# Kernel optimization log

Hardware: AMD Instinct MI355X
Metric: run time of the kernel (lower is better)

## Reference

```python
import jax, jax.numpy as jnp
import numpy as np

B, C, H, W = 8, 512, 64, 64
TEMB = 512
HIDDEN = 1024  # int(C * prompt_hidden_ratio=2.0)
K = C // 2     # max(1, int(C * topk_ratio=0.5))


def silu(x):
    return x * jax.nn.sigmoid(x)


def conv1x1(h, w, b):
    # h: [b,c,hh,ww], w: [out,in], b: [out]
    return jnp.einsum('bchw,oc->bohw', h, w) + b[None, :, None, None]


def setup_inputs() -> dict:
    key = jax.random.key(0)
    ks = jax.random.split(key, 12)
    s = 0.02  # small init so softmax/attention stay well-conditioned
    return {
        'x': jax.random.normal(ks[0], (B, C, H, W), jnp.float32),
        'temb': jax.random.normal(ks[1], (B, TEMB), jnp.float32),
        'w_affine': jax.random.normal(ks[2], (2 * C, TEMB), jnp.float32) * s,
        'b_affine': jnp.zeros((2 * C,), jnp.float32),
        'w_tp': jax.random.normal(ks[3], (C, TEMB), jnp.float32) * s,
        'b_tp': jnp.zeros((C,), jnp.float32),
        'w_m1': jax.random.normal(ks[4], (HIDDEN, 2 * C), jnp.float32) * s,
        'b_m1': jnp.zeros((HIDDEN,), jnp.float32),
        'w_m2': jax.random.normal(ks[5], (C, HIDDEN), jnp.float32) * s,
        'b_m2': jnp.zeros((C,), jnp.float32),
        'wq': jax.random.normal(ks[6], (C, C), jnp.float32) * s,
        'bq': jnp.zeros((C,), jnp.float32),
        'wk': jax.random.normal(ks[7], (C, C), jnp.float32) * s,
        'bk': jnp.zeros((C,), jnp.float32),
        'wv': jax.random.normal(ks[8], (C, C), jnp.float32) * s,
        'bv': jnp.zeros((C,), jnp.float32),
        'wo': jax.random.normal(ks[9], (C, C), jnp.float32) * s,
        'bo': jnp.zeros((C,), jnp.float32),
    }


def reference(x, temb, w_affine, b_affine, w_tp, b_tp, w_m1, b_m1, w_m2, b_m2,
              wq, bq, wk, bk, wv, bv, wo, bo):
    b, c, hgt, wgt = x.shape
    hw = hgt * wgt

    # TimeScaleShift
    temb_act = silu(temb)
    ss = temb_act @ w_affine.T + b_affine              # [b, 2c]
    scale, shift = jnp.split(ss, 2, axis=1)
    h = x * (1.0 + scale[:, :, None, None]) + shift[:, :, None, None]

    # channel prompt
    gap = h.mean(axis=(2, 3))                          # [b, c]
    time_prompt = temb_act @ w_tp.T + b_tp             # [b, c]
    pm = jnp.concatenate([gap, time_prompt], axis=1)   # [b, 2c]
    prompt = silu(pm @ w_m1.T + b_m1) @ w_m2.T + b_m2  # [b, c]

    # top-k channel selection
    _, topk_idx = jax.lax.top_k(prompt, K)             # [b, K] int32

    # q/k/v 1x1 convs, then gather selected channels
    qf = conv1x1(h, wq, bq).reshape(b, c, hw)
    kf = conv1x1(h, wk, bk).reshape(b, c, hw)
    vf = conv1x1(h, wv, bv).reshape(b, c, hw)
    idx3 = topk_idx[:, :, None]
    q = jnp.take_along_axis(qf, idx3, axis=1)          # [b, K, hw]
    k_feat = jnp.take_along_axis(kf, idx3, axis=1)
    v = jnp.take_along_axis(vf, idx3, axis=1)

    # channel attention on the selected subset
    attn = jnp.einsum('bkn,bln->bkl', q, k_feat) * (K ** -0.5)  # [b, K, K]
    attn = jax.nn.softmax(attn, axis=2)
    out = jnp.einsum('bkl,bln->bkn', attn, v)                   # [b, K, hw]

    # scatter back into a zero tensor at the selected channels
    out_full = jax.vmap(
        lambda o, i: jnp.zeros((c, hw), o.dtype).at[i].set(o)
    )(out, topk_idx).reshape(b, c, hgt, wgt)

    return conv1x1(out_full, wo, bo)
```

## Files before the change

### kernel.cpp

```cpp
#include <hip/hip_runtime.h>
#include <hip/hip_bf16.h>
#include <math.h>

typedef __hip_bfloat16 bf16;
typedef __bf16 bf16x8 __attribute__((ext_vector_type(8)));
typedef float f32x4 __attribute__((ext_vector_type(4)));

static __device__ __forceinline__ float b2f(bf16 v) { return __bfloat162float(v); }
static __device__ __forceinline__ bf16 f2b(float v) { return __float2bfloat16(v); }

#define GLOAD16(g, l) __builtin_amdgcn_global_load_lds( \
    (const __attribute__((address_space(1))) void*)(g), \
    (__attribute__((address_space(3))) void*)(l), 16, 0, 0)

#define TM 128
#define TN 64
#define TK 32

template <typename TOUT>
__global__ __launch_bounds__(256) void gemm_bt(
    const bf16* __restrict__ A, size_t sA,
    const bf16* __restrict__ Bt, size_t sB,
    const float* __restrict__ bias, size_t sBias, int hasBias,
    TOUT* __restrict__ D, size_t sD,
    int M, int N, int Kd, int transStore, int NXB)
{
    const int id = blockIdx.x;
    const int bz = id & 7;
    const int slot = id >> 3;
    const int bx = slot % NXB, by = slot / NXB;

    A  += (size_t)bz * sA;
    Bt += (size_t)bz * sB;
    D  += (size_t)bz * sD;
    if (hasBias) bias += (size_t)bz * sBias;

    const int m0 = by * TM, n0 = bx * TN;
    const int t = threadIdx.x, wv = t >> 6, lane = t & 63;
    const int lr = lane & 15, quad = lane >> 4;

    __shared__ bf16 lA[TM * TK];
    __shared__ bf16 lB[TN * TK];

    f32x4 acc[2][4];
#pragma unroll
    for (int i = 0; i < 2; ++i)
#pragma unroll
        for (int j = 0; j < 4; ++j) acc[i][j] = (f32x4){0.f, 0.f, 0.f, 0.f};

    const int srow = lane >> 2, scol = (lane & 3) * 8;
    const bf16* as0 = A  + (size_t)(m0 + wv * 16 + srow) * Kd + scol;
    const bf16* bs0 = Bt + (size_t)(n0 + wv * 16 + srow) * Kd + scol;
    bf16* la0 = lA + wv * 512;
    bf16* lb0 = lB + wv * 512;

    for (int k0 = 0; k0 < Kd; k0 += TK) {
        __syncthreads();
        GLOAD16(as0 + k0, la0);
        GLOAD16(as0 + (size_t)64 * Kd + k0, la0 + 2048);
        GLOAD16(bs0 + k0, lb0);
        __syncthreads();

        bf16x8 af0 = *(const bf16x8*)(lA + (wv * 32 + lr) * 32 + quad * 8);
        bf16x8 af1 = *(const bf16x8*)(lA + (wv * 32 + 16 + lr) * 32 + quad * 8);
#pragma unroll
        for (int j = 0; j < 4; ++j) {
            bf16x8 bfj = *(const bf16x8*)(lB + (j * 16 + lr) * 32 + quad * 8);
            acc[0][j] = __builtin_amdgcn_mfma_f32_16x16x32_bf16(af0, bfj, acc[0][j], 0, 0, 0);
            acc[1][j] = __builtin_amdgcn_mfma_f32_16x16x32_bf16(af1, bfj, acc[1][j], 0, 0, 0);
        }
    }

#pragma unroll
    for (int i = 0; i < 2; ++i) {
        const int mb = m0 + wv * 32 + i * 16 + quad * 4;
#pragma unroll
        for (int r = 0; r < 4; ++r) {
            const int mm = mb + r;
            const float bvv = hasBias ? bias[mm] : 0.f;
#pragma unroll
            for (int j = 0; j < 4; ++j) {
                const int nn = n0 + j * 16 + lr;
                const float v = acc[i][j][r] + bvv;
                const size_t o = transStore ? ((size_t)nn * M + mm)
                                            : ((size_t)mm * N + nn);
                if constexpr (__is_same(TOUT, float)) D[o] = v;
                else                                  D[o] = f2b(v);
            }
        }
    }
}

__global__ __launch_bounds__(256) void k_prep(const float* __restrict__ x,
                                              bf16* __restrict__ xT,
                                              float* __restrict__ xsump)
{
    const int b = blockIdx.z;
    const int c0 = blockIdx.y * 64;
    const int n0 = blockIdx.x * 512;
    const int t = threadIdx.x;
    const int cr = t >> 2;
    const int sub = t & 3;
    __shared__ bf16 tile[64][72];

    const float* xrow = x + ((size_t)b * 512 + c0 + cr) * 4096 + n0 + sub * 16;
    float s = 0.f;

    for (int st = 0; st < 8; ++st) {
        __syncthreads();
        float4 f[4];
#pragma unroll
        for (int q = 0; q < 4; ++q) f[q] = *(const float4*)(xrow + st * 64 + q * 4);
#pragma unroll
        for (int q = 0; q < 4; ++q) {
            s += f[q].x + f[q].y + f[q].z + f[q].w;
            union { bf16 h[4]; uint2 u; } p;
            p.h[0] = f2b(f[q].x); p.h[1] = f2b(f[q].y);
            p.h[2] = f2b(f[q].z); p.h[3] = f2b(f[q].w);
            *(uint2*)&tile[cr][sub * 16 + q * 4] = p.u;
        }
        __syncthreads();
        union { bf16 h[8]; uint4 u; } o0, o1;
#pragma unroll
        for (int i = 0; i < 8; ++i) o0.h[i] = tile[sub * 16 + i][cr];
#pragma unroll
        for (int i = 0; i < 8; ++i) o1.h[i] = tile[sub * 16 + 8 + i][cr];
        bf16* orow = xT + ((size_t)b * 4096 + n0 + st * 64 + cr) * 512 + c0 + sub * 16;
        *(uint4*)(orow)     = o0.u;
        *(uint4*)(orow + 8) = o1.u;
    }
    s += __shfl_down(s, 2);
    s += __shfl_down(s, 1);
    if (sub == 0) xsump[(size_t)blockIdx.x * 4096 + b * 512 + c0 + cr] = s;
}

__global__ __launch_bounds__(256) void gemm_qkv2(
    const bf16* __restrict__ Aall, const bf16* __restrict__ xT,
    const float* __restrict__ bias,
    bf16* __restrict__ qb, bf16* __restrict__ kb, bf16* __restrict__ vT)
{
    const int id = blockIdx.x;
    const int b = id & 7;
    const int slot = id >> 3;
    const int mt = slot % 6;
    const int n0 = (slot / 6) * 128;

    const bf16* A  = Aall + (size_t)b * 393216 + (size_t)mt * 65536;
    const bf16* Bt = xT + (size_t)b * 2097152;
    bias += b * 768 + mt * 128;

    const int t = threadIdx.x, w = t >> 6, lane = t & 63;
    const int lr = lane & 15, quad = lane >> 4;
    const int wr = w >> 1, wc = w & 1;

    __shared__ bf16 lA[128 * 32];
    __shared__ bf16 lB[128 * 32];

    f32x4 acc[4][4];
#pragma unroll
    for (int i = 0; i < 4; ++i)
#pragma unroll
        for (int j = 0; j < 4; ++j) acc[i][j] = (f32x4){0.f, 0.f, 0.f, 0.f};

    const int srow = lane >> 2, scol = (lane & 3) * 8;
    const bf16* as0 = A  + (size_t)(w * 16 + srow) * 512 + scol;
    const bf16* bs0 = Bt + (size_t)(n0 + w * 16 + srow) * 512 + scol;
    bf16* la0 = lA + w * 512;
    bf16* lb0 = lB + w * 512;

    for (int k0 = 0; k0 < 512; k0 += 32) {
        __syncthreads();
        GLOAD16(as0 + k0, la0);
        GLOAD16(as0 + 32768 + k0, la0 + 2048);
        GLOAD16(bs0 + k0, lb0);
        GLOAD16(bs0 + 32768 + k0, lb0 + 2048);
        __syncthreads();

        bf16x8 af[4], bfr[4];
#pragma unroll
        for (int i = 0; i < 4; ++i)
            af[i] = *(const bf16x8*)(lA + (wr * 64 + i * 16 + lr) * 32 + quad * 8);
#pragma unroll
        for (int j = 0; j < 4; ++j)
            bfr[j] = *(const bf16x8*)(lB + (wc * 64 + j * 16 + lr) * 32 + quad * 8);
#pragma unroll
        for (int i = 0; i < 4; ++i)
#pragma unroll
            for (int j = 0; j < 4; ++j)
                acc[i][j] = __builtin_amdgcn_mfma_f32_16x16x32_bf16(af[i], bfr[j], acc[i][j], 0, 0, 0);
    }

#pragma unroll
    for (int i = 0; i < 4; ++i) {
        const int mq = wr * 64 + i * 16 + quad * 4;
#pragma unroll
        for (int r = 0; r < 4; ++r) {
            const int ml = mq + r;
            const float bvv = bias[ml];
            const int mmg = mt * 128 + ml;
            const int mloc = mmg & 255;
#pragma unroll
            for (int j = 0; j < 4; ++j) {
                const int nn = n0 + wc * 64 + j * 16 + lr;
                const float v = acc[i][j][r] + bvv;
                if (mmg < 256)      qb[(size_t)b * 1048576 + (size_t)mloc * 4096 + nn] = f2b(v);
                else if (mmg < 512) kb[(size_t)b * 1048576 + (size_t)mloc * 4096 + nn] = f2b(v);
                else                vT[(size_t)b * 1048576 + (size_t)nn * 256 + mloc] = f2b(v);
            }
        }
    }
}

__global__ __launch_bounds__(256) void gemm_s_splitk(
    const bf16* __restrict__ qb, const bf16* __restrict__ kb,
    float* __restrict__ part)
{
    const int id = blockIdx.x;
    const int b = id & 7;
    const int slot = id >> 3;
    const int s = slot >> 3;
    const int rem = slot & 7;
    const int m0 = (rem >> 2) * TM, n0 = (rem & 3) * TN;

    const bf16* A  = qb + (size_t)b * 1048576;
    const bf16* Bt = kb + (size_t)b * 1048576;

    const int t = threadIdx.x, wv = t >> 6, lane = t & 63;
    const int lr = lane & 15, quad = lane >> 4;

    __shared__ bf16 lA[TM * TK];
    __shared__ bf16 lB[TN * TK];

    f32x4 acc[2][4];
#pragma unroll
    for (int i = 0; i < 2; ++i)
#pragma unroll
        for (int j = 0; j < 4; ++j) acc[i][j] = (f32x4){0.f, 0.f, 0.f, 0.f};

    const int srow = lane >> 2, scol = (lane & 3) * 8;
    const bf16* as0 = A  + (size_t)(m0 + wv * 16 + srow) * 4096 + scol;
    const bf16* bs0 = Bt + (size_t)(n0 + wv * 16 + srow) * 4096 + scol;
    bf16* la0 = lA + wv * 512;
    bf16* lb0 = lB + wv * 512;

    const int kBeg = s * 512, kEnd = kBeg + 512;
    for (int k0 = kBeg; k0 < kEnd; k0 += TK) {
        __syncthreads();
        GLOAD16(as0 + k0, la0);
        GLOAD16(as0 + (size_t)64 * 4096 + k0, la0 + 2048);
        GLOAD16(bs0 + k0, lb0);
        __syncthreads();

        bf16x8 af0 = *(const bf16x8*)(lA + (wv * 32 + lr) * 32 + quad * 8);
        bf16x8 af1 = *(const bf16x8*)(lA + (wv * 32 + 16 + lr) * 32 + quad * 8);
#pragma unroll
        for (int j = 0; j < 4; ++j) {
            bf16x8 bfj = *(const bf16x8*)(lB + (j * 16 + lr) * 32 + quad * 8);
            acc[0][j] = __builtin_amdgcn_mfma_f32_16x16x32_bf16(af0, bfj, acc[0][j], 0, 0, 0);
            acc[1][j] = __builtin_amdgcn_mfma_f32_16x16x32_bf16(af1, bfj, acc[1][j], 0, 0, 0);
        }
    }

    float* dst = part + ((size_t)(s * 8 + b) * 256) * 256;
#pragma unroll
    for (int i = 0; i < 2; ++i) {
        const int mb = m0 + wv * 32 + i * 16 + quad * 4;
#pragma unroll
        for (int r = 0; r < 4; ++r) {
            const int mm = mb + r;
#pragma unroll
            for (int j = 0; j < 4; ++j)
                dst[(size_t)mm * 256 + n0 + j * 16 + lr] = acc[i][j][r];
        }
    }
}


__global__ void k_silu(const float* __restrict__ in, float* __restrict__ out, int n)
{
    int i = blockIdx.x * 256 + threadIdx.x;
    if (i < n) {
        float v = in[i];
        out[i] = v / (1.f + expf(-v));
    }
}

__global__ void k_smallgemm(const float* __restrict__ in, const float* __restrict__ W,
                            const float* __restrict__ bias, float* __restrict__ out,
                            int Mrows, int O, int Kd, int act)
{
    const int gw = (blockIdx.x * 256 + threadIdx.x) >> 6;
    const int lane = threadIdx.x & 63;
    if (gw >= Mrows * O) return;
    const int m = gw / O, o = gw - m * O;
    float s = 0.f;
    for (int k = lane; k < Kd; k += 64)
        s += in[m * Kd + k] * W[(size_t)o * Kd + k];
    for (int off = 32; off; off >>= 1) s += __shfl_down(s, off);
    if (lane == 0) {
        s += bias[o];
        if (act) s = s / (1.f + expf(-s));
        out[m * O + o] = s;
    }
}

__global__ void k_mlp1(const float* __restrict__ ss, const float* __restrict__ xsump,
                       const float* __restrict__ tp, const float* __restrict__ w_m1,
                       const float* __restrict__ b_m1, float* __restrict__ hidden)
{
    const int gw = (blockIdx.x * 256 + threadIdx.x) >> 6;
    const int lane = threadIdx.x & 63;
    if (gw >= 8 * 1024) return;
    const int m = gw >> 10, o = gw & 1023;
    float s = 0.f;
    for (int k = lane; k < 1024; k += 64) {
        float pv;
        if (k < 512) {
            float xs = 0.f;
#pragma unroll
            for (int p = 0; p < 8; ++p) xs += xsump[p * 4096 + m * 512 + k];
            pv = (1.f + ss[m * 1024 + k]) * (xs * (1.f / 4096.f))
                 + ss[m * 1024 + 512 + k];
        } else {
            pv = tp[m * 512 + k - 512];
        }
        s += pv * w_m1[(size_t)o * 1024 + k];
    }
    for (int off = 32; off; off >>= 1) s += __shfl_down(s, off);
    if (lane == 0) {
        s += b_m1[o];
        hidden[m * 1024 + o] = s / (1.f + expf(-s));
    }
}

__global__ void k_topk(const float* __restrict__ prompt, int* __restrict__ idx)
{
    __shared__ float v[512];
    __shared__ int sel[512];
    const int b = blockIdx.x, c = threadIdx.x;
    v[c] = prompt[b * 512 + c];
    __syncthreads();
    const float mv = v[c];
    int rank = 0;
    for (int j = 0; j < 512; ++j) {
        float o = v[j];
        rank += (o > mv) || (o == mv && j < c);
    }
    sel[c] = (rank < 256) ? 1 : 0;
    __syncthreads();
    if (rank < 256) {
        int pos = 0;
        for (int j = 0; j < c; ++j) pos += sel[j];
        idx[b * 256 + pos] = c;
    }
}

__global__ void k_gather(const int* __restrict__ idx, const float* __restrict__ ss,
                         const float* __restrict__ wq, const float* __restrict__ wk,
                         const float* __restrict__ wv, const float* __restrict__ wo,
                         bf16* __restrict__ wqkv_g, bf16* __restrict__ wo_g)
{
    const int b = blockIdx.z;
    const int* id = idx + b * 256;
    const int tid = blockIdx.x * 256 + threadIdx.x;
    {
        const int mat = tid >> 17, r = tid & 131071;
        const int j = r >> 9, c = r & 511;
        const int ch = id[j];
        const float* W = mat == 0 ? wq : (mat == 1 ? wk : wv);
        wqkv_g[(size_t)b * 393216 + tid] = f2b(W[ch * 512 + c] * (1.f + ss[b * 1024 + c]));
    }
    if (tid < 131072) {
        const int o = tid >> 8, j = tid & 255;
        wo_g[(size_t)b * 131072 + tid] = f2b(wo[o * 512 + id[j]]);
    }
}

__global__ void k_biasadj(const int* __restrict__ idx, const float* __restrict__ ss,
                          const float* __restrict__ wq, const float* __restrict__ bq,
                          const float* __restrict__ wk, const float* __restrict__ bk,
                          const float* __restrict__ wv, const float* __restrict__ bv,
                          float* __restrict__ bqkv)
{
    const int gw = (blockIdx.x * 256 + threadIdx.x) >> 6;
    const int lane = threadIdx.x & 63;
    if (gw >= 8 * 768) return;
    const int b = gw / 768, j3 = gw - b * 768;
    const int mat = j3 >> 8, j = j3 & 255;
    const int ch = idx[b * 256 + j];
    const float* W  = mat == 0 ? wq : (mat == 1 ? wk : wv);
    const float* Bb = mat == 0 ? bq : (mat == 1 ? bk : bv);
    const float* shift = ss + b * 1024 + 512;
    float s = 0.f;
    for (int c = lane; c < 512; c += 64)
        s += W[(size_t)ch * 512 + c] * shift[c];
    for (int off = 32; off; off >>= 1) s += __shfl_down(s, off);
    if (lane == 0) bqkv[b * 768 + j3] = Bb[ch] + s;
}

__global__ void k_softmax_red(const float* __restrict__ part, bf16* __restrict__ Pt)
{
    const int row = blockIdx.x;
    const int b = row >> 8, j = row & 255;
    const int t = threadIdx.x;
    const int lane = t & 63, wv = t >> 6;
    __shared__ float redm[4], reds[4];
    float v = 0.f;
#pragma unroll
    for (int s = 0; s < 8; ++s)
        v += part[((size_t)(s * 8 + b) * 256 + j) * 256 + t];
    v *= 0.0625f;
    float m = v;
    for (int off = 32; off; off >>= 1) m = fmaxf(m, __shfl_down(m, off));
    if (lane == 0) redm[wv] = m;
    __syncthreads();
    m = fmaxf(fmaxf(redm[0], redm[1]), fmaxf(redm[2], redm[3]));
    const float e = __expf(v - m);
    float s = e;
    for (int off = 32; off; off >>= 1) s += __shfl_down(s, off);
    if (lane == 0) reds[wv] = s;
    __syncthreads();
    s = reds[0] + reds[1] + reds[2] + reds[3];
    Pt[(size_t)b * 65536 + (size_t)t * 256 + j] = f2b(e / s);
}


extern "C" void kernel_launch(void* const* d_in, const int* in_sizes, int n_in,
                              void* d_out, int out_size, void* d_ws, size_t ws_size,
                              hipStream_t stream)
{
    const float* x        = (const float*)d_in[0];
    const float* temb     = (const float*)d_in[1];
    const float* w_affine = (const float*)d_in[2];
    const float* b_affine = (const float*)d_in[3];
    const float* w_tp     = (const float*)d_in[4];
    const float* b_tp     = (const float*)d_in[5];
    const float* w_m1     = (const float*)d_in[6];
    const float* b_m1     = (const float*)d_in[7];
    const float* w_m2     = (const float*)d_in[8];
    const float* b_m2     = (const float*)d_in[9];
    const float* wq       = (const float*)d_in[10];
    const float* bq       = (const float*)d_in[11];
    const float* wk       = (const float*)d_in[12];
    const float* bk       = (const float*)d_in[13];
    const float* wv       = (const float*)d_in[14];
    const float* bv       = (const float*)d_in[15];
    const float* wo       = (const float*)d_in[16];
    const float* bo       = (const float*)d_in[17];
    float* out = (float*)d_out;

    char* ws = (char*)d_ws;
    size_t off = 0;
    auto alloc = [&](size_t bytes) -> char* {
        char* p = ws + off;
        off += (bytes + 255) & ~(size_t)255;
        return p;
    };

    float* temb_act = (float*)alloc(4096 * 4);
    float* ssb      = (float*)alloc(8192 * 4);
    float* tp       = (float*)alloc(4096 * 4);
    float* xsump    = (float*)alloc((size_t)8 * 4096 * 4);
    float* hidden   = (float*)alloc(8192 * 4);
    float* prompt   = (float*)alloc(4096 * 4);
    int*   idx      = (int*)alloc(2048 * 4);
    bf16*  xT     = (bf16*)alloc((size_t)8 * 4096 * 512 * 2);
    float* part   = (float*)alloc((size_t)8 * 8 * 256 * 256 * 4);
    bf16*  wqkv_g = (bf16*)alloc((size_t)8 * 768 * 512 * 2);
    float* bqkv_g = (float*)alloc(8 * 768 * 4);
    bf16*  wo_g   = (bf16*)alloc((size_t)8 * 512 * 256 * 2);
    bf16*  qb     = (bf16*)alloc((size_t)8 * 256 * 4096 * 2);
    bf16*  kb     = (bf16*)alloc((size_t)8 * 256 * 4096 * 2);
    bf16*  vT     = (bf16*)alloc((size_t)8 * 4096 * 256 * 2);
    bf16*  Pt     = (bf16*)alloc((size_t)8 * 256 * 256 * 2);
    bf16*  W2     = (bf16*)alloc((size_t)8 * 512 * 256 * 2);
    (void)ws_size; (void)n_in; (void)in_sizes; (void)out_size;

    k_prep<<<dim3(8, 8, 8), 256, 0, stream>>>(x, xT, xsump);
    k_silu<<<16, 256, 0, stream>>>(temb, temb_act, 4096);
    k_smallgemm<<<2048, 256, 0, stream>>>(temb_act, w_affine, b_affine, ssb, 8, 1024, 512, 0);
    k_smallgemm<<<1024, 256, 0, stream>>>(temb_act, w_tp, b_tp, tp, 8, 512, 512, 0);
    k_mlp1<<<2048, 256, 0, stream>>>(ssb, xsump, tp, w_m1, b_m1, hidden);
    k_smallgemm<<<1024, 256, 0, stream>>>(hidden, w_m2, b_m2, prompt, 8, 512, 1024, 0);
    k_topk<<<8, 512, 0, stream>>>(prompt, idx);
    k_gather<<<dim3(1536, 1, 8), 256, 0, stream>>>(idx, ssb, wq, wk, wv, wo, wqkv_g, wo_g);
    k_biasadj<<<1536, 256, 0, stream>>>(idx, ssb, wq, bq, wk, bk, wv, bv, bqkv_g);
    gemm_qkv2<<<1536, 256, 0, stream>>>(wqkv_g, xT, bqkv_g, qb, kb, vT);
    gemm_s_splitk<<<512, 256, 0, stream>>>(qb, kb, part);
    k_softmax_red<<<2048, 256, 0, stream>>>(part, Pt);
    gemm_bt<bf16><<<128, 256, 0, stream>>>(wo_g, 131072, Pt, 65536,
                                           nullptr, 0, 0,
                                           W2, 131072, 512, 256, 256, 0, 4);
    gemm_bt<float><<<2048, 256, 0, stream>>>(W2, 131072, vT, 1048576,
                                             bo, 0, 1,
                                             out, 2097152, 512, 4096, 256, 0, 64);
}
```

Measured before the change: 339.9 us.

## Double-buffer LDS tiles and XOR-swizzle layout in bf16 GEMM kernels

Three MFMA GEMM kernels now prefetch the next K-tile into a second LDS buffer while computing on the current one, which removes one barrier per iteration. The LDS column placement is also XOR-swizzled by row to reduce bank conflicts on the 16-byte fragment reads. This doubles shared memory per block, which may lower occupancy. It also relies on the barrier waiting for the asynchronous global-to-LDS loads.

Measured after the change: 341.4 us. No clear change (+0.4%).

```diff
diff --git a/kernel.cpp b/kernel.cpp
--- a/kernel.cpp
+++ b/kernel.cpp
@@ -12,6 +12,7 @@
 #define GLOAD16(g, l) __builtin_amdgcn_global_load_lds( \
     (const __attribute__((address_space(1))) void*)(g), \
     (__attribute__((address_space(3))) void*)(l), 16, 0, 0)
+
 
 #define TM 128
 #define TN 64
@@ -38,9 +39,10 @@
     const int m0 = by * TM, n0 = bx * TN;
     const int t = threadIdx.x, wv = t >> 6, lane = t & 63;
     const int lr = lane & 15, quad = lane >> 4;
-
-    __shared__ bf16 lA[TM * TK];
-    __shared__ bf16 lB[TN * TK];
+    const int qx8 = (quad ^ ((lr >> 1) & 3)) * 8;
+
+    __shared__ bf16 lA[2][TM * TK];
+    __shared__ bf16 lB[2][TN * TK];
 
     f32x4 acc[2][4];
 #pragma unroll
@@ -48,27 +50,36 @@
 #pragma unroll
         for (int j = 0; j < 4; ++j) acc[i][j] = (f32x4){0.f, 0.f, 0.f, 0.f};
 
-    const int srow = lane >> 2, scol = (lane & 3) * 8;
+    const int srow = lane >> 2;
+    const int scol = ((lane & 3) ^ ((lane >> 3) & 3)) * 8;
     const bf16* as0 = A  + (size_t)(m0 + wv * 16 + srow) * Kd + scol;
     const bf16* bs0 = Bt + (size_t)(n0 + wv * 16 + srow) * Kd + scol;
-    bf16* la0 = lA + wv * 512;
-    bf16* lb0 = lB + wv * 512;
-
+
+    GLOAD16(as0, &lA[0][wv * 512]);
+    GLOAD16(as0 + (size_t)64 * Kd, &lA[0][wv * 512 + 2048]);
+    GLOAD16(bs0, &lB[0][wv * 512]);
+    __syncthreads();
+
+    int cur = 0;
     for (int k0 = 0; k0 < Kd; k0 += TK) {
-        __syncthreads();
-        GLOAD16(as0 + k0, la0);
-        GLOAD16(as0 + (size_t)64 * Kd + k0, la0 + 2048);
-        GLOAD16(bs0 + k0, lb0);
-        __syncthreads();
-
-        bf16x8 af0 = *(const bf16x8*)(lA + (wv * 32 + lr) * 32 + quad * 8);
-        bf16x8 af1 = *(const bf16x8*)(lA + (wv * 32 + 16 + lr) * 32 + quad * 8);
+        const int kn = k0 + TK;
+        if (kn < Kd) {
+            GLOAD16(as0 + kn, &lA[cur ^ 1][wv * 512]);
+            GLOAD16(as0 + (size_t)64 * Kd + kn, &lA[cur ^ 1][wv * 512 + 2048]);
+            GLOAD16(bs0 + kn, &lB[cur ^ 1][wv * 512]);
+        }
+        const bf16* bA = lA[cur];
+        const bf16* bB = lB[cur];
+        bf16x8 af0 = *(const bf16x8*)(bA + (wv * 32 + lr) * 32 + qx8);
+        bf16x8 af1 = *(const bf16x8*)(bA + (wv * 32 + 16 + lr) * 32 + qx8);
 #pragma unroll
         for (int j = 0; j < 4; ++j) {
-            bf16x8 bfj = *(const bf16x8*)(lB + (j * 16 + lr) * 32 + quad * 8);
+            bf16x8 bfj = *(const bf16x8*)(bB + (j * 16 + lr) * 32 + qx8);
             acc[0][j] = __builtin_amdgcn_mfma_f32_16x16x32_bf16(af0, bfj, acc[0][j], 0, 0, 0);
             acc[1][j] = __builtin_amdgcn_mfma_f32_16x16x32_bf16(af1, bfj, acc[1][j], 0, 0, 0);
         }
+        __syncthreads();
+        cur ^= 1;
     }
 
 #pragma unroll
@@ -152,9 +163,10 @@
     const int t = threadIdx.x, w = t >> 6, lane = t & 63;
     const int lr = lane & 15, quad = lane >> 4;
     const int wr = w >> 1, wc = w & 1;
-
-    __shared__ bf16 lA[128 * 32];
-    __shared__ bf16 lB[128 * 32];
+    const int qx8 = (quad ^ ((lr >> 1) & 3)) * 8;
+
+    __shared__ bf16 lA[2][128 * 32];
+    __shared__ bf16 lB[2][128 * 32];
 
     f32x4 acc[4][4];
 #pragma unroll
@@ -162,32 +174,42 @@
 #pragma unroll
         for (int j = 0; j < 4; ++j) acc[i][j] = (f32x4){0.f, 0.f, 0.f, 0.f};
 
-    const int srow = lane >> 2, scol = (lane & 3) * 8;
+    const int srow = lane >> 2;
+    const int scol = ((lane & 3) ^ ((lane >> 3) & 3)) * 8;
     const bf16* as0 = A  + (size_t)(w * 16 + srow) * 512 + scol;
     const bf16* bs0 = Bt + (size_t)(n0 + w * 16 + srow) * 512 + scol;
-    bf16* la0 = lA + w * 512;
-    bf16* lb0 = lB + w * 512;
-
+
+    GLOAD16(as0, &lA[0][w * 512]);
+    GLOAD16(as0 + 32768, &lA[0][w * 512 + 2048]);
+    GLOAD16(bs0, &lB[0][w * 512]);
+    GLOAD16(bs0 + 32768, &lB[0][w * 512 + 2048]);
+    __syncthreads();
+
+    int cur = 0;
     for (int k0 = 0; k0 < 512; k0 += 32) {
-        __syncthreads();
-        GLOAD16(as0 + k0, la0);
-        GLOAD16(as0 + 32768 + k0, la0 + 2048);
-        GLOAD16(bs0 + k0, lb0);
-        GLOAD16(bs0 + 32768 + k0, lb0 + 2048);
-        __syncthreads();
-
+        const int kn = k0 + 32;
+        if (kn < 512) {
+            GLOAD16(as0 + kn, &lA[cur ^ 1][w * 512]);
+            GLOAD16(as0 + 32768 + kn, &lA[cur ^ 1][w * 512 + 2048]);
+            GLOAD16(bs0 + kn, &lB[cur ^ 1][w * 512]);
+            GLOAD16(bs0 + 32768 + kn, &lB[cur ^ 1][w * 512 + 2048]);
+        }
+        const bf16* bA = lA[cur];
+        const bf16* bB = lB[cur];
         bf16x8 af[4], bfr[4];
 #pragma unroll
         for (int i = 0; i < 4; ++i)
-            af[i] = *(const bf16x8*)(lA + (wr * 64 + i * 16 + lr) * 32 + quad * 8);
+            af[i] = *(const bf16x8*)(bA + (wr * 64 + i * 16 + lr) * 32 + qx8);
 #pragma unroll
         for (int j = 0; j < 4; ++j)
-            bfr[j] = *(const bf16x8*)(lB + (wc * 64 + j * 16 + lr) * 32 + quad * 8);
+            bfr[j] = *(const bf16x8*)(bB + (wc * 64 + j * 16 + lr) * 32 + qx8);
 #pragma unroll
         for (int i = 0; i < 4; ++i)
 #pragma unroll
             for (int j = 0; j < 4; ++j)
                 acc[i][j] = __builtin_amdgcn_mfma_f32_16x16x32_bf16(af[i], bfr[j], acc[i][j], 0, 0, 0);
+        __syncthreads();
+        cur ^= 1;
     }
 
 #pragma unroll
@@ -227,9 +249,10 @@
 
     const int t = threadIdx.x, wv = t >> 6, lane = t & 63;
     const int lr = lane & 15, quad = lane >> 4;
-
-    __shared__ bf16 lA[TM * TK];
-    __shared__ bf16 lB[TN * TK];
+    const int qx8 = (quad ^ ((lr >> 1) & 3)) * 8;
+
+    __shared__ bf16 lA[2][TM * TK];
+    __shared__ bf16 lB[2][TN * TK];
 
     f32x4 acc[2][4];
 #pragma unroll
@@ -237,28 +260,38 @@
 #pragma unroll
         for (int j = 0; j < 4; ++j) acc[i][j] = (f32x4){0.f, 0.f, 0.f, 0.f};
 
-    const int srow = lane >> 2, scol = (lane & 3) * 8;
+    const int srow = lane >> 2;
+    const int scol = ((lane & 3) ^ ((lane >> 3) & 3)) * 8;
     const bf16* as0 = A  + (size_t)(m0 + wv * 16 + srow) * 4096 + scol;
     const bf16* bs0 = Bt + (size_t)(n0 + wv * 16 + srow) * 4096 + scol;
-    bf16* la0 = lA + wv * 512;
-    bf16* lb0 = lB + wv * 512;
 
     const int kBeg = s * 512, kEnd = kBeg + 512;
+
+    GLOAD16(as0 + kBeg, &lA[0][wv * 512]);
+    GLOAD16(as0 + (size_t)64 * 4096 + kBeg, &lA[0][wv * 512 + 2048]);
+    GLOAD16(bs0 + kBeg, &lB[0][wv * 512]);
+    __syncthreads();
+
+    int cur = 0;
     for (int k0 = kBeg; k0 < kEnd; k0 += TK) {
-        __syncthreads();
-        GLOAD16(as0 + k0, la0);
-        GLOAD16(as0 + (size_t)64 * 4096 + k0, la0 + 2048);
-        GLOAD16(bs0 + k0, lb0);
-        __syncthreads();
-
-        bf16x8 af0 = *(const bf16x8*)(lA + (wv * 32 + lr) * 32 + quad * 8);
-        bf16x8 af1 = *(const bf16x8*)(lA + (wv * 32 + 16 + lr) * 32 + quad * 8);
+        const int kn = k0 + TK;
+        if (kn < kEnd) {
+            GLOAD16(as0 + kn, &lA[cur ^ 1][wv * 512]);
+            GLOAD16(as0 + (size_t)64 * 4096 + kn, &lA[cur ^ 1][wv * 512 + 2048]);
+            GLOAD16(bs0 + kn, &lB[cur ^ 1][wv * 512]);
+        }
+        const bf16* bA = lA[cur];
+        const bf16* bB = lB[cur];
+        bf16x8 af0 = *(const bf16x8*)(bA + (wv * 32 + lr) * 32 + qx8);
+        bf16x8 af1 = *(const bf16x8*)(bA + (wv * 32 + 16 + lr) * 32 + qx8);
 #pragma unroll
         for (int j = 0; j < 4; ++j) {
-            bf16x8 bfj = *(const bf16x8*)(lB + (j * 16 + lr) * 32 + quad * 8);
+            bf16x8 bfj = *(const bf16x8*)(bB + (j * 16 + lr) * 32 + qx8);
             acc[0][j] = __builtin_amdgcn_mfma_f32_16x16x32_bf16(af0, bfj, acc[0][j], 0, 0, 0);
             acc[1][j] = __builtin_amdgcn_mfma_f32_16x16x32_bf16(af1, bfj, acc[1][j], 0, 0, 0);
         }
+        __syncthreads();
+        cur ^= 1;
     }
 
     float* dst = part + ((size_t)(s * 8 + b) * 256) * 256;
```

## Restructure GEMMs to keep full-K A tile in LDS and stream B from registers

Applied to the files above, without the earlier changes.

Replaces the tiled LDS double-sync GEMMs with kernels that load the whole A panel (32 or 64 rows by full K) into XOR-swizzled LDS once, then read B fragments straight from global memory into registers. This removes the per-K-step barriers and the LDS staging of B. The QKV GEMM moves to 512-thread blocks with larger N tiles, and the split-K S GEMM and output GEMMs share one templated kernel. The temb SiLU is also folded into the small GEMM, which drops one launch. In exchange, B loads are uncoalesced direct global reads, and the large LDS footprint limits occupancy.

Result: slower. 394.2 us (+16.0%).

```diff
diff --git a/kernel.cpp b/kernel.cpp
--- a/kernel.cpp
+++ b/kernel.cpp
@@ -13,34 +13,50 @@
     (const __attribute__((address_space(1))) void*)(g), \
     (__attribute__((address_space(3))) void*)(l), 16, 0, 0)
 
-#define TM 128
-#define TN 64
-#define TK 32
-
-template <typename TOUT>
-__global__ __launch_bounds__(256) void gemm_bt(
-    const bf16* __restrict__ A, size_t sA,
-    const bf16* __restrict__ Bt, size_t sB,
+template <typename TOUT, int KSL>
+__global__ __launch_bounds__(256) void gemm_ws(
+    const bf16* __restrict__ A, size_t sA, int lda,
+    const bf16* __restrict__ Bt, size_t sB, int ldb,
     const float* __restrict__ bias, size_t sBias, int hasBias,
-    TOUT* __restrict__ D, size_t sD,
-    int M, int N, int Kd, int transStore, int NXB)
-{
+    TOUT* __restrict__ D, size_t sD, size_t sDs,
+    int N, int NMT, int NNC)
+{
+    constexpr int KSTEPS = KSL / 32;
     const int id = blockIdx.x;
     const int bz = id & 7;
-    const int slot = id >> 3;
-    const int bx = slot % NXB, by = slot / NXB;
-
-    A  += (size_t)bz * sA;
-    Bt += (size_t)bz * sB;
-    D  += (size_t)bz * sD;
-    if (hasBias) bias += (size_t)bz * sBias;
-
-    const int m0 = by * TM, n0 = bx * TN;
+    int slot = id >> 3;
+    const int mt = slot % NMT; slot /= NMT;
+    const int nc = slot % NNC;
+    const int ks = slot / NNC;
+    const int n0 = nc * 256;
+
+    A  += (size_t)bz * sA + (size_t)(mt * 32) * lda + (size_t)ks * KSL;
+    Bt += (size_t)bz * sB + (size_t)ks * KSL;
+    D  += (size_t)bz * sD + (size_t)ks * sDs;
+    if (hasBias) bias += (size_t)bz * sBias + mt * 32;
+
     const int t = threadIdx.x, wv = t >> 6, lane = t & 63;
     const int lr = lane & 15, quad = lane >> 4;
-
-    __shared__ bf16 lA[TM * TK];
-    __shared__ bf16 lB[TN * TK];
+    const int xr7 = lr & 7;
+
+    __shared__ bf16 lA[32 * KSL];
+
+    if constexpr (KSL == 512) {
+#pragma unroll
+        for (int rr = 0; rr < 8; ++rr) {
+            const int r = wv * 8 + rr;
+            GLOAD16(A + (size_t)r * lda + ((lane ^ (r & 7)) << 3), &lA[r * 512]);
+        }
+    } else {
+#pragma unroll
+        for (int rr = 0; rr < 4; ++rr) {
+            const int rb = wv * 8 + rr * 2;
+            const int rl = rb + (lane >> 5);
+            GLOAD16(A + (size_t)rl * lda + (((lane & 31) ^ (rl & 7)) << 3),
+                    &lA[rb * 256]);
+        }
+    }
+    __syncthreads();
 
     f32x4 acc[2][4];
 #pragma unroll
@@ -48,44 +64,113 @@
 #pragma unroll
         for (int j = 0; j < 4; ++j) acc[i][j] = (f32x4){0.f, 0.f, 0.f, 0.f};
 
-    const int srow = lane >> 2, scol = (lane & 3) * 8;
-    const bf16* as0 = A  + (size_t)(m0 + wv * 16 + srow) * Kd + scol;
-    const bf16* bs0 = Bt + (size_t)(n0 + wv * 16 + srow) * Kd + scol;
-    bf16* la0 = lA + wv * 512;
-    bf16* lb0 = lB + wv * 512;
-
-    for (int k0 = 0; k0 < Kd; k0 += TK) {
-        __syncthreads();
-        GLOAD16(as0 + k0, la0);
-        GLOAD16(as0 + (size_t)64 * Kd + k0, la0 + 2048);
-        GLOAD16(bs0 + k0, lb0);
-        __syncthreads();
-
-        bf16x8 af0 = *(const bf16x8*)(lA + (wv * 32 + lr) * 32 + quad * 8);
-        bf16x8 af1 = *(const bf16x8*)(lA + (wv * 32 + 16 + lr) * 32 + quad * 8);
+    const bf16* bp[4];
+#pragma unroll
+    for (int j = 0; j < 4; ++j)
+        bp[j] = Bt + (size_t)(n0 + wv * 64 + j * 16 + lr) * ldb + quad * 8;
+
+#pragma unroll 2
+    for (int k2 = 0; k2 < KSTEPS; ++k2) {
+        const int ao = ((((k2 << 2) | quad) ^ xr7) << 3);
+        bf16x8 bfr[4];
+#pragma unroll
+        for (int j = 0; j < 4; ++j)
+            bfr[j] = *(const bf16x8*)(bp[j] + k2 * 32);
+        bf16x8 af0 = *(const bf16x8*)&lA[lr * KSL + ao];
+        bf16x8 af1 = *(const bf16x8*)&lA[(16 + lr) * KSL + ao];
 #pragma unroll
         for (int j = 0; j < 4; ++j) {
-            bf16x8 bfj = *(const bf16x8*)(lB + (j * 16 + lr) * 32 + quad * 8);
-            acc[0][j] = __builtin_amdgcn_mfma_f32_16x16x32_bf16(af0, bfj, acc[0][j], 0, 0, 0);
-            acc[1][j] = __builtin_amdgcn_mfma_f32_16x16x32_bf16(af1, bfj, acc[1][j], 0, 0, 0);
+            acc[0][j] = __builtin_amdgcn_mfma_f32_16x16x32_bf16(af0, bfr[j], acc[0][j], 0, 0, 0);
+            acc[1][j] = __builtin_amdgcn_mfma_f32_16x16x32_bf16(af1, bfr[j], acc[1][j], 0, 0, 0);
         }
     }
 
 #pragma unroll
     for (int i = 0; i < 2; ++i) {
-        const int mb = m0 + wv * 32 + i * 16 + quad * 4;
 #pragma unroll
         for (int r = 0; r < 4; ++r) {
-            const int mm = mb + r;
-            const float bvv = hasBias ? bias[mm] : 0.f;
+            const int ml = i * 16 + quad * 4 + r;
+            const int mrow = mt * 32 + ml;
+            const float bvv = hasBias ? bias[ml] : 0.f;
 #pragma unroll
             for (int j = 0; j < 4; ++j) {
-                const int nn = n0 + j * 16 + lr;
+                const int nn = n0 + wv * 64 + j * 16 + lr;
                 const float v = acc[i][j][r] + bvv;
-                const size_t o = transStore ? ((size_t)nn * M + mm)
-                                            : ((size_t)mm * N + nn);
-                if constexpr (__is_same(TOUT, float)) D[o] = v;
-                else                                  D[o] = f2b(v);
+                if constexpr (__is_same(TOUT, float)) D[(size_t)mrow * N + nn] = v;
+                else                                  D[(size_t)mrow * N + nn] = f2b(v);
+            }
+        }
+    }
+}
+
+__global__ __launch_bounds__(512, 4) void gemm_qkv3(
+    const bf16* __restrict__ Aall, const bf16* __restrict__ xT,
+    const float* __restrict__ bias,
+    bf16* __restrict__ qb, bf16* __restrict__ kb, bf16* __restrict__ vT)
+{
+    const int id = blockIdx.x;
+    const int b = id & 7;
+    const int slot = id >> 3;
+    const int mt = slot % 12;
+    const int n0 = (slot / 12) * 512;
+
+    const bf16* A  = Aall + (size_t)b * 393216 + (size_t)(mt * 64) * 512;
+    const bf16* Bt = xT + (size_t)b * 2097152;
+    bias += b * 768 + mt * 64;
+
+    const int t = threadIdx.x, w = t >> 6, lane = t & 63;
+    const int lr = lane & 15, quad = lane >> 4;
+    const int xr7 = lr & 7;
+
+    __shared__ bf16 lA[64 * 512];
+
+#pragma unroll
+    for (int rr = 0; rr < 8; ++rr) {
+        const int r = w * 8 + rr;
+        GLOAD16(A + (size_t)r * 512 + ((lane ^ (r & 7)) << 3), &lA[r * 512]);
+    }
+    __syncthreads();
+
+    f32x4 acc[4][4];
+#pragma unroll
+    for (int i = 0; i < 4; ++i)
+#pragma unroll
+        for (int j = 0; j < 4; ++j) acc[i][j] = (f32x4){0.f, 0.f, 0.f, 0.f};
+
+    const bf16* bp0 = Bt + (size_t)(n0 + w * 64 + lr) * 512 + quad * 8;
+
+    for (int k2 = 0; k2 < 16; ++k2) {
+        const int ao = ((((k2 << 2) | quad) ^ xr7) << 3);
+        bf16x8 bfr[4];
+#pragma unroll
+        for (int j = 0; j < 4; ++j)
+            bfr[j] = *(const bf16x8*)(bp0 + (size_t)j * 8192 + k2 * 32);
+        bf16x8 af[4];
+#pragma unroll
+        for (int i = 0; i < 4; ++i)
+            af[i] = *(const bf16x8*)&lA[(i * 16 + lr) * 512 + ao];
+#pragma unroll
+        for (int i = 0; i < 4; ++i)
+#pragma unroll
+            for (int j = 0; j < 4; ++j)
+                acc[i][j] = __builtin_amdgcn_mfma_f32_16x16x32_bf16(af[i], bfr[j], acc[i][j], 0, 0, 0);
+    }
+
+#pragma unroll
+    for (int i = 0; i < 4; ++i) {
+#pragma unroll
+        for (int r = 0; r < 4; ++r) {
+            const int ml = i * 16 + quad * 4 + r;
+            const int mmg = mt * 64 + ml;
+            const int mloc = mmg & 255;
+            const float bvv = bias[ml];
+#pragma unroll
+            for (int j = 0; j < 4; ++j) {
+                const int nn = n0 + w * 64 + j * 16 + lr;
+                const float v = acc[i][j][r] + bvv;
+                if (mt < 4)       qb[(size_t)b * 1048576 + (size_t)mloc * 4096 + nn] = f2b(v);
+                else if (mt < 8)  kb[(size_t)b * 1048576 + (size_t)mloc * 4096 + nn] = f2b(v);
+                else              vT[(size_t)b * 1048576 + (size_t)nn * 256 + mloc] = f2b(v);
             }
         }
     }
@@ -134,168 +219,21 @@
     if (sub == 0) xsump[(size_t)blockIdx.x * 4096 + b * 512 + c0 + cr] = s;
 }
 
-__global__ __launch_bounds__(256) void gemm_qkv2(
-    const bf16* __restrict__ Aall, const bf16* __restrict__ xT,
-    const float* __restrict__ bias,
-    bf16* __restrict__ qb, bf16* __restrict__ kb, bf16* __restrict__ vT)
-{
-    const int id = blockIdx.x;
-    const int b = id & 7;
-    const int slot = id >> 3;
-    const int mt = slot % 6;
-    const int n0 = (slot / 6) * 128;
-
-    const bf16* A  = Aall + (size_t)b * 393216 + (size_t)mt * 65536;
-    const bf16* Bt = xT + (size_t)b * 2097152;
-    bias += b * 768 + mt * 128;
-
-    const int t = threadIdx.x, w = t >> 6, lane = t & 63;
-    const int lr = lane & 15, quad = lane >> 4;
-    const int wr = w >> 1, wc = w & 1;
-
-    __shared__ bf16 lA[128 * 32];
-    __shared__ bf16 lB[128 * 32];
-
-    f32x4 acc[4][4];
-#pragma unroll
-    for (int i = 0; i < 4; ++i)
-#pragma unroll
-        for (int j = 0; j < 4; ++j) acc[i][j] = (f32x4){0.f, 0.f, 0.f, 0.f};
-
-    const int srow = lane >> 2, scol = (lane & 3) * 8;
-    const bf16* as0 = A  + (size_t)(w * 16 + srow) * 512 + scol;
-    const bf16* bs0 = Bt + (size_t)(n0 + w * 16 + srow) * 512 + scol;
-    bf16* la0 = lA + w * 512;
-    bf16* lb0 = lB + w * 512;
-
-    for (int k0 = 0; k0 < 512; k0 += 32) {
-        __syncthreads();
-        GLOAD16(as0 + k0, la0);
-        GLOAD16(as0 + 32768 + k0, la0 + 2048);
-        GLOAD16(bs0 + k0, lb0);
-        GLOAD16(bs0 + 32768 + k0, lb0 + 2048);
-        __syncthreads();
-
-        bf16x8 af[4], bfr[4];
-#pragma unroll
-        for (int i = 0; i < 4; ++i)
-            af[i] = *(const bf16x8*)(lA + (wr * 64 + i * 16 + lr) * 32 + quad * 8);
-#pragma unroll
-        for (int j = 0; j < 4; ++j)
-            bfr[j] = *(const bf16x8*)(lB + (wc * 64 + j * 16 + lr) * 32 + quad * 8);
-#pragma unroll
-        for (int i = 0; i < 4; ++i)
-#pragma unroll
-            for (int j = 0; j < 4; ++j)
-                acc[i][j] = __builtin_amdgcn_mfma_f32_16x16x32_bf16(af[i], bfr[j], acc[i][j], 0, 0, 0);
-    }
-
-#pragma unroll
-    for (int i = 0; i < 4; ++i) {
-        const int mq = wr * 64 + i * 16 + quad * 4;
-#pragma unroll
-        for (int r = 0; r < 4; ++r) {
-            const int ml = mq + r;
-            const float bvv = bias[ml];
-            const int mmg = mt * 128 + ml;
-            const int mloc = mmg & 255;
-#pragma unroll
-            for (int j = 0; j < 4; ++j) {
-                const int nn = n0 + wc * 64 + j * 16 + lr;
-                const float v = acc[i][j][r] + bvv;
-                if (mmg < 256)      qb[(size_t)b * 1048576 + (size_t)mloc * 4096 + nn] = f2b(v);
-                else if (mmg < 512) kb[(size_t)b * 1048576 + (size_t)mloc * 4096 + nn] = f2b(v);
-                else                vT[(size_t)b * 1048576 + (size_t)nn * 256 + mloc] = f2b(v);
-            }
-        }
-    }
-}
-
-__global__ __launch_bounds__(256) void gemm_s_splitk(
-    const bf16* __restrict__ qb, const bf16* __restrict__ kb,
-    float* __restrict__ part)
-{
-    const int id = blockIdx.x;
-    const int b = id & 7;
-    const int slot = id >> 3;
-    const int s = slot >> 3;
-    const int rem = slot & 7;
-    const int m0 = (rem >> 2) * TM, n0 = (rem & 3) * TN;
-
-    const bf16* A  = qb + (size_t)b * 1048576;
-    const bf16* Bt = kb + (size_t)b * 1048576;
-
-    const int t = threadIdx.x, wv = t >> 6, lane = t & 63;
-    const int lr = lane & 15, quad = lane >> 4;
-
-    __shared__ bf16 lA[TM * TK];
-    __shared__ bf16 lB[TN * TK];
-
-    f32x4 acc[2][4];
-#pragma unroll
-    for (int i = 0; i < 2; ++i)
-#pragma unroll
-        for (int j = 0; j < 4; ++j) acc[i][j] = (f32x4){0.f, 0.f, 0.f, 0.f};
-
-    const int srow = lane >> 2, scol = (lane & 3) * 8;
-    const bf16* as0 = A  + (size_t)(m0 + wv * 16 + srow) * 4096 + scol;
-    const bf16* bs0 = Bt + (size_t)(n0 + wv * 16 + srow) * 4096 + scol;
-    bf16* la0 = lA + wv * 512;
-    bf16* lb0 = lB + wv * 512;
-
-    const int kBeg = s * 512, kEnd = kBeg + 512;
-    for (int k0 = kBeg; k0 < kEnd; k0 += TK) {
-        __syncthreads();
-        GLOAD16(as0 + k0, la0);
-        GLOAD16(as0 + (size_t)64 * 4096 + k0, la0 + 2048);
-        GLOAD16(bs0 + k0, lb0);
-        __syncthreads();
-
-        bf16x8 af0 = *(const bf16x8*)(lA + (wv * 32 + lr) * 32 + quad * 8);
-        bf16x8 af1 = *(const bf16x8*)(lA + (wv * 32 + 16 + lr) * 32 + quad * 8);
-#pragma unroll
-        for (int j = 0; j < 4; ++j) {
-            bf16x8 bfj = *(const bf16x8*)(lB + (j * 16 + lr) * 32 + quad * 8);
-            acc[0][j] = __builtin_amdgcn_mfma_f32_16x16x32_bf16(af0, bfj, acc[0][j], 0, 0, 0);
-            acc[1][j] = __builtin_amdgcn_mfma_f32_16x16x32_bf16(af1, bfj, acc[1][j], 0, 0, 0);
-        }
-    }
-
-    float* dst = part + ((size_t)(s * 8 + b) * 256) * 256;
-#pragma unroll
-    for (int i = 0; i < 2; ++i) {
-        const int mb = m0 + wv * 32 + i * 16 + quad * 4;
-#pragma unroll
-        for (int r = 0; r < 4; ++r) {
-            const int mm = mb + r;
-#pragma unroll
-            for (int j = 0; j < 4; ++j)
-                dst[(size_t)mm * 256 + n0 + j * 16 + lr] = acc[i][j][r];
-        }
-    }
-}
-
-
-__global__ void k_silu(const float* __restrict__ in, float* __restrict__ out, int n)
-{
-    int i = blockIdx.x * 256 + threadIdx.x;
-    if (i < n) {
-        float v = in[i];
-        out[i] = v / (1.f + expf(-v));
-    }
-}
 
 __global__ void k_smallgemm(const float* __restrict__ in, const float* __restrict__ W,
                             const float* __restrict__ bias, float* __restrict__ out,
-                            int Mrows, int O, int Kd, int act)
+                            int Mrows, int O, int Kd, int act, int inAct)
 {
     const int gw = (blockIdx.x * 256 + threadIdx.x) >> 6;
     const int lane = threadIdx.x & 63;
     if (gw >= Mrows * O) return;
     const int m = gw / O, o = gw - m * O;
     float s = 0.f;
-    for (int k = lane; k < Kd; k += 64)
-        s += in[m * Kd + k] * W[(size_t)o * Kd + k];
+    for (int k = lane; k < Kd; k += 64) {
+        float iv = in[m * Kd + k];
+        if (inAct) iv = iv / (1.f + expf(-iv));
+        s += iv * W[(size_t)o * Kd + k];
+    }
     for (int off = 32; off; off >>= 1) s += __shfl_down(s, off);
     if (lane == 0) {
         s += bias[o];
@@ -457,7 +395,6 @@
         return p;
     };
 
-    float* temb_act = (float*)alloc(4096 * 4);
     float* ssb      = (float*)alloc(8192 * 4);
     float* tp       = (float*)alloc(4096 * 4);
     float* xsump    = (float*)alloc((size_t)8 * 4096 * 4);
@@ -477,21 +414,30 @@
     (void)ws_size; (void)n_in; (void)in_sizes; (void)out_size;
 
     k_prep<<<dim3(8, 8, 8), 256, 0, stream>>>(x, xT, xsump);
-    k_silu<<<16, 256, 0, stream>>>(temb, temb_act, 4096);
-    k_smallgemm<<<2048, 256, 0, stream>>>(temb_act, w_affine, b_affine, ssb, 8, 1024, 512, 0);
-    k_smallgemm<<<1024, 256, 0, stream>>>(temb_act, w_tp, b_tp, tp, 8, 512, 512, 0);
+    k_smallgemm<<<2048, 256, 0, stream>>>(temb, w_affine, b_affine, ssb, 8, 1024, 512, 0, 1);
+    k_smallgemm<<<1024, 256, 0, stream>>>(temb, w_tp, b_tp, tp, 8, 512, 512, 0, 1);
     k_mlp1<<<2048, 256, 0, stream>>>(ssb, xsump, tp, w_m1, b_m1, hidden);
-    k_smallgemm<<<1024, 256, 0, stream>>>(hidden, w_m2, b_m2, prompt, 8, 512, 1024, 0);
+    k_smallgemm<<<1024, 256, 0, stream>>>(hidden, w_m2, b_m2, prompt, 8, 512, 1024, 0, 0);
     k_topk<<<8, 512, 0, stream>>>(prompt, idx);
     k_gather<<<dim3(1536, 1, 8), 256, 0, stream>>>(idx, ssb, wq, wk, wv, wo, wqkv_g, wo_g);
     k_biasadj<<<1536, 256, 0, stream>>>(idx, ssb, wq, bq, wk, bk, wv, bv, bqkv_g);
-    gemm_qkv2<<<1536, 256, 0, stream>>>(wqkv_g, xT, bqkv_g, qb, kb, vT);
-    gemm_s_splitk<<<512, 256, 0, stream>>>(qb, kb, part);
+
+    gemm_qkv3<<<768, 512, 0, stream>>>(wqkv_g, xT, bqkv_g, qb, kb, vT);
+
+    gemm_ws<float, 512><<<512, 256, 0, stream>>>(
+        qb, 1048576, 4096, kb, 1048576, 4096,
+        nullptr, 0, 0,
+        part, 65536, 524288, 256, 8, 1);
+
     k_softmax_red<<<2048, 256, 0, stream>>>(part, Pt);
-    gemm_bt<bf16><<<128, 256, 0, stream>>>(wo_g, 131072, Pt, 65536,
-                                           nullptr, 0, 0,
-                                           W2, 131072, 512, 256, 256, 0, 4);
-    gemm_bt<float><<<2048, 256, 0, stream>>>(W2, 131072, vT, 1048576,
-                                             bo, 0, 1,
-                                             out, 2097152, 512, 4096, 256, 0, 64);
-}
+
+    gemm_ws<bf16, 256><<<128, 256, 0, stream>>>(
+        wo_g, 131072, 256, Pt, 65536, 256,
+        nullptr, 0, 0,
+        W2, 131072, 0, 256, 16, 1);
+
+    gemm_ws<float, 256><<<2048, 256, 0, stream>>>(
+        W2, 131072, 256, vT, 1048576, 256,
+        bo, 0, 1,
+        out, 2097152, 0, 4096, 16, 16);
+}
```
